# Performance work log

Measured on AMD Instinct MI355X. Metric: run time of the kernel, lower is better.

## Reference

```python
import jax, jax.numpy as jnp
import numpy as np

N_NODES = 100000
N_EDGES = 3200000
N_GRAPHS = 1024
F_IN = 78
H = 128
BN_EPS = 1e-5


def setup_inputs() -> dict:
    key = jax.random.key(0)
    ks = jax.random.split(key, 10)
    x = jax.random.normal(ks[0], (N_NODES, F_IN), dtype=jnp.float32)
    edge_index = jax.random.randint(ks[1], (2, N_EDGES), 0, N_NODES, dtype=jnp.int64)
    batch = jnp.sort(jax.random.randint(ks[2], (N_NODES,), 0, N_GRAPHS, dtype=jnp.int64))
    s_in = 1.0 / np.sqrt(F_IN)
    s_h = 1.0 / np.sqrt(H)
    return {
        "x": x,
        "edge_index": edge_index,
        "batch": batch,
        "W1_0": jax.random.normal(ks[3], (F_IN, H), dtype=jnp.float32) * s_in,
        "b1_0": jnp.zeros((H,), jnp.float32),
        "W2_0": jax.random.normal(ks[4], (H, H), dtype=jnp.float32) * s_h,
        "b2_0": jnp.zeros((H,), jnp.float32),
        "W1": jax.random.normal(ks[5], (4, H, H), dtype=jnp.float32) * s_h,
        "b1": jnp.zeros((4, H), jnp.float32),
        "W2": jax.random.normal(ks[6], (4, H, H), dtype=jnp.float32) * s_h,
        "b2": jnp.zeros((4, H), jnp.float32),
        "gamma": jnp.ones((5, H), jnp.float32),
        "beta": jnp.zeros((5, H), jnp.float32),
        "Wf": jax.random.normal(ks[7], (2 * H, H), dtype=jnp.float32) * (1.0 / np.sqrt(2 * H)),
        "bf": jnp.zeros((H,), jnp.float32),
    }


def _gin_layer(x, src, dst, W1l, b1l, W2l, b2l, g, bta):
    # GINConv, eps=0: h_i = x_i + sum_{(j->i) in E} x_j, then 2-layer MLP
    agg = jax.ops.segment_sum(x[src], dst, num_segments=N_NODES)  # [N, F]
    h = x + agg
    h = jax.nn.relu(h @ W1l + b1l) @ W2l + b2l
    h = jax.nn.relu(h)
    # BatchNorm1d (training mode: biased batch statistics)
    mu = jnp.mean(h, axis=0)
    var = jnp.mean(jnp.square(h - mu), axis=0)
    return (h - mu) * (g / jnp.sqrt(var + BN_EPS)) + bta


def reference(x, edge_index, batch, W1_0, b1_0, W2_0, b2_0, W1, b1, W2, b2, gamma, beta, Wf, bf):
    src, dst = edge_index[0], edge_index[1]
    # layer 0 (no residual: dims 78 -> 128)
    h = _gin_layer(x, src, dst, W1_0, b1_0, W2_0, b2_0, gamma[0], beta[0])
    # layers 1..4 with residual
    for i in range(4):
        h_new = _gin_layer(h, src, dst, W1[i], b1[i], W2[i], b2[i], gamma[i + 1], beta[i + 1])
        h = h + h_new
    # global mean pool
    sums = jax.ops.segment_sum(h, batch, num_segments=N_GRAPHS)  # [G, H]
    counts = jax.ops.segment_sum(jnp.ones((h.shape[0],), h.dtype), batch, num_segments=N_GRAPHS)
    mean_pool = sums / jnp.maximum(counts, 1.0)[:, None]
    # global max pool (empty segments -> 0)
    max_pool = jax.ops.segment_max(h, batch, num_segments=N_GRAPHS)
    max_pool = jnp.where(counts[:, None] > 0, max_pool, 0.0)
    combined = jnp.concatenate([mean_pool, max_pool], axis=1)  # [G, 2H]
    return combined @ Wf + bf
```

## Files before the change

kernel.cpp:

```cpp
#include <hip/hip_runtime.h>
#include <float.h>

#define N_NODES 100000
#define N_EDGES 3200000
#define N_GRAPHS 1024
#define F_IN 78
#define H 128
#define BN_EPS 1e-5f

#define BK_SHIFT 7
#define BK_NODES 128
#define NBUCKETS ((N_NODES + BK_NODES - 1) / BK_NODES)

#define P3_BLOCKS 800
#define P3_CHUNK 4000

using short8 = __attribute__((ext_vector_type(8))) short;
using f32x4v = __attribute__((ext_vector_type(4))) float;

__device__ __forceinline__ unsigned short f2bf(float f) {
    unsigned int u = __float_as_uint(f);
    unsigned int r = (u + 0x7fffu + ((u >> 16) & 1u)) >> 16;
    return (unsigned short)r;
}
__device__ __forceinline__ float bf_lo(unsigned int u) { return __uint_as_float(u << 16); }
__device__ __forceinline__ float bf_hi(unsigned int u) { return __uint_as_float(u & 0xffff0000u); }


__global__ __launch_bounds__(256) void k_hist(const int* __restrict__ dst,
                                              int* __restrict__ bofs) {
    __shared__ int lcnt[NBUCKETS];
    for (int i = threadIdx.x; i < NBUCKETS; i += 256) lcnt[i] = 0;
    __syncthreads();
    int base = blockIdx.x * P3_CHUNK;
    for (int j = threadIdx.x; j < P3_CHUNK; j += 256)
        atomicAdd(&lcnt[dst[base + j] >> BK_SHIFT], 1);
    __syncthreads();
    for (int i = threadIdx.x; i < NBUCKETS; i += 256)
        bofs[blockIdx.x * NBUCKETS + i] = lcnt[i];
}

__global__ __launch_bounds__(1024) void k_scan2(int* __restrict__ bofs,
                                                int* __restrict__ bbase,
                                                int* __restrict__ row_start) {
    __shared__ int tot[1024];
    int b = threadIdx.x;
    int run = 0;
    if (b < NBUCKETS) {
#pragma unroll 8
        for (int blk = 0; blk < P3_BLOCKS; ++blk) {
            int v = bofs[blk * NBUCKETS + b];
            bofs[blk * NBUCKETS + b] = run;
            run += v;
        }
    }
    tot[threadIdx.x] = (b < NBUCKETS) ? run : 0;
    __syncthreads();
    if (threadIdx.x == 0) {
        int acc = 0;
        for (int i = 0; i < NBUCKETS; ++i) { int t = tot[i]; tot[i] = acc; acc += t; }
    }
    __syncthreads();
    if (b < NBUCKETS) bbase[b] = tot[b];
    if (threadIdx.x == 0) {
        bbase[NBUCKETS] = N_EDGES;
        row_start[N_NODES] = N_EDGES;
    }
}

__global__ __launch_bounds__(256) void k_p3b(const int* __restrict__ src,
                                             const int* __restrict__ dst,
                                             const int* __restrict__ bofs,
                                             const int* __restrict__ bbase,
                                             unsigned int* __restrict__ ebuf) {
    __shared__ int cur[NBUCKETS];
    for (int i = threadIdx.x; i < NBUCKETS; i += 256)
        cur[i] = bbase[i] + bofs[blockIdx.x * NBUCKETS + i];
    __syncthreads();
    int base = blockIdx.x * P3_CHUNK;
    for (int j = threadIdx.x; j < P3_CHUNK; j += 256) {
        int d = dst[base + j];
        int p = atomicAdd(&cur[d >> BK_SHIFT], 1);
        ebuf[p] = ((unsigned int)src[base + j] << 7) | (unsigned int)(d & (BK_NODES - 1));
    }
}

__global__ __launch_bounds__(256) void k_p4(const int* __restrict__ bbase,
                                            const unsigned int* __restrict__ ebuf,
                                            int* __restrict__ esrc,
                                            int* __restrict__ row_start) {
    __shared__ int cur[BK_NODES];
    __shared__ int start[BK_NODES];
    int b = blockIdx.x;
    int nodeBase = b << BK_SHIFT;
    int nLocal = min(BK_NODES, N_NODES - nodeBase);
    if (threadIdx.x < BK_NODES) cur[threadIdx.x] = 0;
    __syncthreads();
    int s = bbase[b], e = bbase[b + 1];
    for (int p = s + threadIdx.x; p < e; p += 256)
        atomicAdd(&cur[ebuf[p] & (BK_NODES - 1)], 1);
    __syncthreads();
    if (threadIdx.x == 0) {
        int run = s;
        for (int i = 0; i < nLocal; ++i) { start[i] = run; run += cur[i]; }
    }
    __syncthreads();
    if (threadIdx.x < nLocal) {
        row_start[nodeBase + threadIdx.x] = start[threadIdx.x];
        cur[threadIdx.x] = start[threadIdx.x];
    }
    __syncthreads();
    for (int p = s + threadIdx.x; p < e; p += 256) {
        unsigned int ed = ebuf[p];
        int q = atomicAdd(&cur[ed & (BK_NODES - 1)], 1);
        esrc[q] = (int)(ed >> 7);
    }
}


__global__ void k_cast_x(const float* __restrict__ x, unsigned short* __restrict__ xb) {
    int i = blockIdx.x * blockDim.x + threadIdx.x;
    if (i >= N_NODES * 96) return;
    int node = i / 96;
    int c = i - node * 96;
    float v = (c < F_IN) ? x[(size_t)node * F_IN + c] : 0.f;
    xb[i] = f2bf(v);
}

__global__ void k_cast_w(const float* __restrict__ W2_0, const float* __restrict__ W1,
                         const float* __restrict__ W2, unsigned short* __restrict__ Wt) {
    int i = blockIdx.x * blockDim.x + threadIdx.x;
    if (i >= 9 * H * H) return;
    int w = i >> 14, r = i & 16383;
    int n = r >> 7, k = r & 127;
    const float* s = (w == 0) ? W2_0 : (w <= 4 ? W1 + (w - 1) * H * H : W2 + (w - 5) * H * H);
    Wt[i] = f2bf(s[k * H + n]);
}

__global__ void k_cast_w0(const float* __restrict__ W1_0, unsigned short* __restrict__ Wt0) {
    int i = blockIdx.x * blockDim.x + threadIdx.x;
    if (i >= H * 96) return;
    int n = i / 96, k = i - n * 96;
    Wt0[i] = f2bf((k < F_IN) ? W1_0[k * H + n] : 0.f);
}


__global__ void k_gather96(const unsigned int* __restrict__ xw,
                           const int* __restrict__ row_start, const int* __restrict__ esrc,
                           unsigned int* __restrict__ out) {
    int wave = threadIdx.x >> 6;
    int lane = threadIdx.x & 63;
    int node = blockIdx.x * 4 + wave;
    int s = row_start[node], e = row_start[node + 1];
    bool act = lane < 48;
    unsigned int su = act ? xw[node * 48 + lane] : 0u;
    float aA[8], aB[8];
#pragma unroll
    for (int j = 0; j < 8; ++j) { aA[j] = 0.f; aB[j] = 0.f; }
    aA[0] = bf_lo(su); aB[0] = bf_hi(su);
    int p = s;
    for (; p + 16 <= e; p += 16) {
        int idx[16];
#pragma unroll
        for (int j = 0; j < 16; ++j) idx[j] = esrc[p + j];
        unsigned int u[16];
#pragma unroll
        for (int j = 0; j < 16; ++j) u[j] = act ? xw[idx[j] * 48 + lane] : 0u;
#pragma unroll
        for (int j = 0; j < 16; ++j) { aA[j & 7] += bf_lo(u[j]); aB[j & 7] += bf_hi(u[j]); }
    }
    for (; p + 4 <= e; p += 4) {
        int i0 = esrc[p], i1 = esrc[p + 1], i2 = esrc[p + 2], i3 = esrc[p + 3];
        unsigned int u0 = act ? xw[i0 * 48 + lane] : 0u;
        unsigned int u1 = act ? xw[i1 * 48 + lane] : 0u;
        unsigned int u2 = act ? xw[i2 * 48 + lane] : 0u;
        unsigned int u3 = act ? xw[i3 * 48 + lane] : 0u;
        aA[0] += bf_lo(u0); aB[0] += bf_hi(u0); aA[1] += bf_lo(u1); aB[1] += bf_hi(u1);
        aA[2] += bf_lo(u2); aB[2] += bf_hi(u2); aA[3] += bf_lo(u3); aB[3] += bf_hi(u3);
    }
    for (; p < e; ++p) {
        unsigned int u = act ? xw[esrc[p] * 48 + lane] : 0u;
        aA[0] += bf_lo(u); aB[0] += bf_hi(u);
    }
    if (act) {
        float rx = ((aA[0] + aA[1]) + (aA[2] + aA[3])) + ((aA[4] + aA[5]) + (aA[6] + aA[7]));
        float ry = ((aB[0] + aB[1]) + (aB[2] + aB[3])) + ((aB[4] + aB[5]) + (aB[6] + aB[7]));
        out[node * 48 + lane] = (unsigned int)f2bf(rx) | ((unsigned int)f2bf(ry) << 16);
    }
}

__global__ void k_gather128b(const unsigned int* __restrict__ hw,
                             const int* __restrict__ row_start, const int* __restrict__ esrc,
                             unsigned int* __restrict__ aggb) {
    int wave = threadIdx.x >> 6;
    int lane = threadIdx.x & 63;
    int node = blockIdx.x * 4 + wave;
    int s = row_start[node], e = row_start[node + 1];
    unsigned int su = hw[node * 64 + lane];
    float aA[8], aB[8];
#pragma unroll
    for (int j = 0; j < 8; ++j) { aA[j] = 0.f; aB[j] = 0.f; }
    aA[0] = bf_lo(su); aB[0] = bf_hi(su);
    int p = s;
    for (; p + 16 <= e; p += 16) {
        int idx[16];
#pragma unroll
        for (int j = 0; j < 16; ++j) idx[j] = esrc[p + j];
        unsigned int u[16];
#pragma unroll
        for (int j = 0; j < 16; ++j) u[j] = hw[idx[j] * 64 + lane];
#pragma unroll
        for (int j = 0; j < 16; ++j) { aA[j & 7] += bf_lo(u[j]); aB[j & 7] += bf_hi(u[j]); }
    }
    for (; p + 4 <= e; p += 4) {
        int i0 = esrc[p], i1 = esrc[p + 1], i2 = esrc[p + 2], i3 = esrc[p + 3];
        unsigned int u0 = hw[i0 * 64 + lane];
        unsigned int u1 = hw[i1 * 64 + lane];
        unsigned int u2 = hw[i2 * 64 + lane];
        unsigned int u3 = hw[i3 * 64 + lane];
        aA[0] += bf_lo(u0); aB[0] += bf_hi(u0); aA[1] += bf_lo(u1); aB[1] += bf_hi(u1);
        aA[2] += bf_lo(u2); aB[2] += bf_hi(u2); aA[3] += bf_lo(u3); aB[3] += bf_hi(u3);
    }
    for (; p < e; ++p) {
        unsigned int u = hw[esrc[p] * 64 + lane];
        aA[0] += bf_lo(u); aB[0] += bf_hi(u);
    }
    float rx = ((aA[0] + aA[1]) + (aA[2] + aA[3])) + ((aA[4] + aA[5]) + (aA[6] + aA[7]));
    float ry = ((aB[0] + aB[1]) + (aB[2] + aB[3])) + ((aB[4] + aB[5]) + (aB[6] + aB[7]));
    aggb[node * 64 + lane] = (unsigned int)f2bf(rx) | ((unsigned int)f2bf(ry) << 16);
}


template <int NK>
__global__ __launch_bounds__(256) void k_mfma1t(const short* __restrict__ A,
                                                const short* __restrict__ Wt,
                                                const float* __restrict__ bias,
                                                unsigned short* __restrict__ out) {
    const int K = NK * 32;
    int wave = threadIdx.x >> 6, lane = threadIdx.x & 63;
    int r0 = blockIdx.x * 64 + wave * 16;
    int lm = lane & 15, lk = lane >> 4;
    int arow = r0 + lm;
    if (arow >= N_NODES) arow = N_NODES - 1;
    const short8* Arow = (const short8*)(A + (size_t)arow * K);
    f32x4v acc[8];
#pragma unroll
    for (int n = 0; n < 8; ++n) {
        float bv = bias[n * 16 + lm];
        acc[n] = (f32x4v){bv, bv, bv, bv};
    }
#pragma unroll
    for (int ks = 0; ks < NK; ++ks) {
        short8 af = Arow[ks * 4 + lk];
#pragma unroll
        for (int n = 0; n < 8; ++n) {
            const short8* Brow = (const short8*)(Wt + (size_t)(n * 16 + lm) * K);
            short8 bfr = Brow[ks * 4 + lk];
            acc[n] = __builtin_amdgcn_mfma_f32_16x16x32_bf16(af, bfr, acc[n], 0, 0, 0);
        }
    }
#pragma unroll
    for (int n = 0; n < 8; ++n) {
        int col = n * 16 + lm;
#pragma unroll
        for (int rg = 0; rg < 4; ++rg) {
            int r = r0 + lk * 4 + rg;
            if (r < N_NODES) {
                float v = fmaxf(acc[n][rg], 0.f);
                out[(size_t)r * H + col] = f2bf(v);
            }
        }
    }
}

__global__ __launch_bounds__(256) void k_mfma2(const short* __restrict__ A,
                                               const short* __restrict__ Wt,
                                               const float* __restrict__ bias,
                                               unsigned short* __restrict__ out,
                                               float* __restrict__ gsum,
                                               float* __restrict__ gss) {
    __shared__ float lsum[H], lss[H];
    if (threadIdx.x < H) { lsum[threadIdx.x] = 0.f; lss[threadIdx.x] = 0.f; }
    __syncthreads();
    int wave = threadIdx.x >> 6, lane = threadIdx.x & 63;
    int r0 = blockIdx.x * 64 + wave * 16;
    int lm = lane & 15, lk = lane >> 4;
    int arow = r0 + lm;
    if (arow >= N_NODES) arow = N_NODES - 1;
    const short8* Arow = (const short8*)(A + (size_t)arow * H);
    f32x4v acc[8];
#pragma unroll
    for (int n = 0; n < 8; ++n) {
        float bv = bias[n * 16 + lm];
        acc[n] = (f32x4v){bv, bv, bv, bv};
    }
#pragma unroll
    for (int ks = 0; ks < 4; ++ks) {
        short8 af = Arow[ks * 4 + lk];
#pragma unroll
        for (int n = 0; n < 8; ++n) {
            const short8* Brow = (const short8*)(Wt + (size_t)(n * 16 + lm) * H);
            short8 bfr = Brow[ks * 4 + lk];
            acc[n] = __builtin_amdgcn_mfma_f32_16x16x32_bf16(af, bfr, acc[n], 0, 0, 0);
        }
    }
#pragma unroll
    for (int n = 0; n < 8; ++n) {
        int col = n * 16 + lm;
        float s = 0.f, q = 0.f;
#pragma unroll
        for (int rg = 0; rg < 4; ++rg) {
            int r = r0 + lk * 4 + rg;
            if (r < N_NODES) {
                float v = fmaxf(acc[n][rg], 0.f);
                out[(size_t)r * H + col] = f2bf(v);
                s += v;
                q += v * v;
            }
        }
        atomicAdd(&lsum[col], s);
        atomicAdd(&lss[col], q);
    }
    __syncthreads();
    if (threadIdx.x < H) {
        atomicAdd(&gsum[threadIdx.x], lsum[threadIdx.x]);
        atomicAdd(&gss[threadIdx.x], lss[threadIdx.x]);
    }
}


__global__ void k_bnfinal(float* __restrict__ gsum, float* __restrict__ gss,
                          const float* __restrict__ gamma, const float* __restrict__ beta,
                          float* __restrict__ scale, float* __restrict__ shift) {
    int c = threadIdx.x;
    const float inv_n = 1.f / (float)N_NODES;
    float sv = gsum[c], qv = gss[c];
    gsum[c] = 0.f;
    gss[c] = 0.f;
    float mu = sv * inv_n;
    float var = fmaxf(qv * inv_n - mu * mu, 0.f);
    float sc = gamma[c] * rsqrtf(var + BN_EPS);
    scale[c] = sc;
    shift[c] = beta[c] - mu * sc;
}

template <bool RES, bool WB>
__global__ void k_bnapply(const uint2* __restrict__ vb, const float* __restrict__ scale,
                          const float* __restrict__ shift, float* __restrict__ h,
                          uint2* __restrict__ hb) {
    int idx = blockIdx.x * blockDim.x + threadIdx.x;
    if (idx >= N_NODES * H / 4) return;
    int c4 = idx & 31;
    uint2 pv = vb[idx];
    float4 val = make_float4(bf_lo(pv.x), bf_hi(pv.x), bf_lo(pv.y), bf_hi(pv.y));
    float4 sc = reinterpret_cast<const float4*>(scale)[c4];
    float4 sh = reinterpret_cast<const float4*>(shift)[c4];
    float4 r;
    r.x = val.x * sc.x + sh.x;
    r.y = val.y * sc.y + sh.y;
    r.z = val.z * sc.z + sh.z;
    r.w = val.w * sc.w + sh.w;
    if (RES) {
        float4 hv = reinterpret_cast<float4*>(h)[idx];
        r.x += hv.x; r.y += hv.y; r.z += hv.z; r.w += hv.w;
    }
    reinterpret_cast<float4*>(h)[idx] = r;
    if (WB) {
        uint2 pk;
        pk.x = (unsigned int)f2bf(r.x) | ((unsigned int)f2bf(r.y) << 16);
        pk.y = (unsigned int)f2bf(r.z) | ((unsigned int)f2bf(r.w) << 16);
        hb[idx] = pk;
    }
}


__global__ void k_bounds(const int* __restrict__ batch, int* __restrict__ row_begin) {
    int i = blockIdx.x * blockDim.x + threadIdx.x;
    if (i >= N_NODES) return;
    int bi = batch[i];
    int bp = (i == 0) ? -1 : batch[i - 1];
    for (int g = bp + 1; g <= bi; ++g) row_begin[g] = i;
    if (i == N_NODES - 1) {
        for (int g = bi + 1; g <= N_GRAPHS; ++g) row_begin[g] = N_NODES;
    }
}

__global__ void k_pool(const float* __restrict__ h, const int* __restrict__ row_begin,
                       float* __restrict__ pooled) {
    int g = blockIdx.x;
    int c = threadIdx.x;
    int s = row_begin[g], e = row_begin[g + 1];
    float sum = 0.f, mx = -FLT_MAX;
    for (int i = s; i < e; ++i) {
        float v = h[(size_t)i * H + c];
        sum += v;
        mx = fmaxf(mx, v);
    }
    int cnt = e - s;
    pooled[g * 256 + c]       = (cnt > 0) ? sum / (float)cnt : 0.f;
    pooled[g * 256 + 128 + c] = (cnt > 0) ? mx : 0.f;
}

__global__ void k_final(const float* __restrict__ pooled, const float* __restrict__ Wf,
                        const float* __restrict__ bf, float* __restrict__ out) {
    __shared__ float ps[256];
    int g = blockIdx.x, c = threadIdx.x;
    ps[c] = pooled[g * 256 + c];
    ps[128 + c] = pooled[g * 256 + 128 + c];
    __syncthreads();
    float acc = bf[c];
#pragma unroll 8
    for (int k = 0; k < 256; ++k) acc += ps[k] * Wf[k * H + c];
    out[g * H + c] = acc;
}


extern "C" void kernel_launch(void* const* d_in, const int* in_sizes, int n_in,
                              void* d_out, int out_size, void* d_ws, size_t ws_size,
                              hipStream_t stream) {
    const float* x     = (const float*)d_in[0];
    const int*   ei    = (const int*)d_in[1];
    const int*   src   = ei;
    const int*   dst   = ei + N_EDGES;
    const int*   batch = (const int*)d_in[2];
    const float* W1_0  = (const float*)d_in[3];
    const float* b1_0  = (const float*)d_in[4];
    const float* W2_0  = (const float*)d_in[5];
    const float* b2_0  = (const float*)d_in[6];
    const float* W1    = (const float*)d_in[7];
    const float* b1    = (const float*)d_in[8];
    const float* W2    = (const float*)d_in[9];
    const float* b2    = (const float*)d_in[10];
    const float* gamma = (const float*)d_in[11];
    const float* beta  = (const float*)d_in[12];
    const float* Wf    = (const float*)d_in[13];
    const float* bf    = (const float*)d_in[14];
    float* out = (float*)d_out;

    char* ws = (char*)d_ws;
    size_t off = 0;
    auto alloc = [&](size_t bytes) -> void* {
        void* p = ws + off;
        off = (off + bytes + 255) & ~(size_t)255;
        return p;
    };

    float* h    = (float*)alloc((size_t)N_NODES * H * 4);
    uint2* hb   = (uint2*)alloc((size_t)N_NODES * H * 2);
    unsigned int*   aggb  = (unsigned int*)alloc((size_t)N_NODES * H * 2);
    unsigned short* act1b = (unsigned short*)alloc((size_t)N_NODES * H * 2);
    unsigned short* act2b = (unsigned short*)alloc((size_t)N_NODES * H * 2);
    unsigned short* xb    = (unsigned short*)alloc((size_t)N_NODES * 96 * 2);
    unsigned int*   agg0b = (unsigned int*)alloc((size_t)N_NODES * 48 * 4);
    unsigned short* Wtall = (unsigned short*)alloc((size_t)9 * H * H * 2);
    unsigned short* Wt0   = (unsigned short*)alloc((size_t)H * 96 * 2);
    int* row_start = (int*)alloc((size_t)(N_NODES + 1) * 4);
    int* esrc      = (int*)alloc((size_t)N_EDGES * 4);
    unsigned int* ebuf = (unsigned int*)alloc((size_t)N_EDGES * 4);
    int* bofs      = (int*)alloc((size_t)P3_BLOCKS * NBUCKETS * 4);
    int* bbase     = (int*)alloc((size_t)(NBUCKETS + 1) * 4);
    float* gsum  = (float*)alloc(H * 4);
    float* gss   = (float*)alloc(H * 4);
    float* scale = (float*)alloc(H * 4);
    float* shift = (float*)alloc(H * 4);
    int* row_begin = (int*)alloc((size_t)(N_GRAPHS + 1) * 4);
    float* pooled  = (float*)alloc((size_t)N_GRAPHS * 256 * 4);

    k_cast_x<<<(N_NODES * 96 + 255) / 256, 256, 0, stream>>>(x, xb);
    k_cast_w<<<(9 * H * H + 255) / 256, 256, 0, stream>>>(W2_0, W1, W2, Wtall);
    k_cast_w0<<<(H * 96 + 255) / 256, 256, 0, stream>>>(W1_0, Wt0);

    k_hist<<<P3_BLOCKS, 256, 0, stream>>>(dst, bofs);
    k_scan2<<<1, 1024, 0, stream>>>(bofs, bbase, row_start);
    k_p3b<<<P3_BLOCKS, 256, 0, stream>>>(src, dst, bofs, bbase, ebuf);
    k_p4<<<NBUCKETS, 256, 0, stream>>>(bbase, ebuf, esrc, row_start);

    hipMemsetAsync(gsum, 0, H * 4, stream);
    hipMemsetAsync(gss, 0, H * 4, stream);

    const int mfma_grid = (N_NODES + 63) / 64;

    k_gather96<<<N_NODES / 4, 256, 0, stream>>>((const unsigned int*)xb, row_start, esrc, agg0b);
    k_mfma1t<3><<<mfma_grid, 256, 0, stream>>>((const short*)agg0b, (const short*)Wt0,
                                               b1_0, act1b);
    k_mfma2<<<mfma_grid, 256, 0, stream>>>((const short*)act1b, (const short*)Wtall, b2_0,
                                           act2b, gsum, gss);
    k_bnfinal<<<1, 128, 0, stream>>>(gsum, gss, gamma, beta, scale, shift);
    k_bnapply<false, true><<<N_NODES * H / 4 / 256, 256, 0, stream>>>((const uint2*)act2b,
                                                                      scale, shift, h, hb);

    for (int l = 0; l < 4; ++l) {
        k_gather128b<<<N_NODES / 4, 256, 0, stream>>>((const unsigned int*)hb, row_start,
                                                      esrc, aggb);
        k_mfma1t<4><<<mfma_grid, 256, 0, stream>>>((const short*)aggb,
                                                   (const short*)(Wtall + (1 + l) * H * H),
                                                   b1 + l * H, act1b);
        k_mfma2<<<mfma_grid, 256, 0, stream>>>((const short*)act1b,
                                               (const short*)(Wtall + (5 + l) * H * H),
                                               b2 + l * H, act2b, gsum, gss);
        k_bnfinal<<<1, 128, 0, stream>>>(gsum, gss, gamma + (l + 1) * H, beta + (l + 1) * H,
                                         scale, shift);
        if (l < 3) {
            k_bnapply<true, true><<<N_NODES * H / 4 / 256, 256, 0, stream>>>((const uint2*)act2b,
                                                                             scale, shift, h, hb);
        } else {
            k_bnapply<true, false><<<N_NODES * H / 4 / 256, 256, 0, stream>>>((const uint2*)act2b,
                                                                              scale, shift, h, hb);
        }
    }

    k_bounds<<<(N_NODES + 255) / 256, 256, 0, stream>>>(batch, row_begin);
    k_pool<<<N_GRAPHS, 128, 0, stream>>>(h, row_begin, pooled);
    k_final<<<N_GRAPHS, 128, 0, stream>>>(pooled, Wf, bf, out);
}
```

Baseline: 1.420 ms.

## Fuse MLP GEMMs via LDS, parallelize bucket scan, fold last BN into pooling

Merges the two per-layer MFMA GEMM kernels into one kernel. The ReLU'd first-layer activations stay in XOR-swizzled shared memory instead of being written to and read back from global memory. The single-block column scan is split into a many-block per-bucket scan plus a small totals scan. The final BatchNorm-apply pass is dropped and its scale/shift plus residual are applied inside the pooling kernel. The costs are 16KB more LDS per block, which may lower occupancy, and one extra kernel launch for the scan.

Result: faster. 1.272 ms (-10.4%).

```diff
diff --git a/kernel.cpp b/kernel.cpp
--- a/kernel.cpp
+++ b/kernel.cpp
@@ -25,6 +25,7 @@
 }
 __device__ __forceinline__ float bf_lo(unsigned int u) { return __uint_as_float(u << 16); }
 __device__ __forceinline__ float bf_hi(unsigned int u) { return __uint_as_float(u & 0xffff0000u); }
+__device__ __forceinline__ float bf1(unsigned short u) { return __uint_as_float((unsigned int)u << 16); }
 
 
 __global__ __launch_bounds__(256) void k_hist(const int* __restrict__ dst,
@@ -40,29 +41,50 @@
         bofs[blockIdx.x * NBUCKETS + i] = lcnt[i];
 }
 
-__global__ __launch_bounds__(1024) void k_scan2(int* __restrict__ bofs,
-                                                int* __restrict__ bbase,
-                                                int* __restrict__ row_start) {
+__global__ __launch_bounds__(256) void k_scan_a(int* __restrict__ bofs,
+                                                int* __restrict__ btot) {
+    __shared__ int part[256];
+    int b = blockIdx.x, t = threadIdx.x;
+    int val[4];
+#pragma unroll
+    for (int j = 0; j < 4; ++j) {
+        int idx = t * 4 + j;
+        val[j] = (idx < P3_BLOCKS) ? bofs[idx * NBUCKETS + b] : 0;
+    }
+    part[t] = val[0] + val[1] + val[2] + val[3];
+    __syncthreads();
+    if (t == 0) {
+        int run = 0;
+        for (int u = 0; u < 256; ++u) { int tmp = part[u]; part[u] = run; run += tmp; }
+        btot[b] = run;
+    }
+    __syncthreads();
+    int off = part[t];
+#pragma unroll
+    for (int j = 0; j < 4; ++j) {
+        int idx = t * 4 + j;
+        if (idx < P3_BLOCKS) {
+            int tmp = val[j];
+            bofs[idx * NBUCKETS + b] = off;
+            off += tmp;
+        }
+    }
+}
+
+__global__ __launch_bounds__(1024) void k_scan_b(const int* __restrict__ btot,
+                                                 int* __restrict__ bbase,
+                                                 int* __restrict__ row_start) {
     __shared__ int tot[1024];
-    int b = threadIdx.x;
-    int run = 0;
-    if (b < NBUCKETS) {
-#pragma unroll 8
-        for (int blk = 0; blk < P3_BLOCKS; ++blk) {
-            int v = bofs[blk * NBUCKETS + b];
-            bofs[blk * NBUCKETS + b] = run;
-            run += v;
-        }
-    }
-    tot[threadIdx.x] = (b < NBUCKETS) ? run : 0;
-    __syncthreads();
-    if (threadIdx.x == 0) {
+    int t = threadIdx.x;
+    tot[t] = (t < NBUCKETS) ? btot[t] : 0;
+    __syncthreads();
+    if (t == 0) {
         int acc = 0;
-        for (int i = 0; i < NBUCKETS; ++i) { int t = tot[i]; tot[i] = acc; acc += t; }
-    }
-    __syncthreads();
-    if (b < NBUCKETS) bbase[b] = tot[b];
-    if (threadIdx.x == 0) {
+        for (int i = 0; i < NBUCKETS; ++i) { int v = tot[i]; tot[i] = acc; acc += v; }
+    }
+    __syncthreads();
+    if (t < NBUCKETS) bbase[t] = tot[t];
+    if (t == 0) {
         bbase[NBUCKETS] = N_EDGES;
         row_start[N_NODES] = N_EDGES;
     }
@@ -231,88 +253,79 @@
 }
 
 
-template <int NK>
-__global__ __launch_bounds__(256) void k_mfma1t(const short* __restrict__ A,
-                                                const short* __restrict__ Wt,
-                                                const float* __restrict__ bias,
-                                                unsigned short* __restrict__ out) {
-    const int K = NK * 32;
+template <int NK1>
+__global__ __launch_bounds__(256) void k_mlp(const short* __restrict__ A,
+                                             const short* __restrict__ Wt1,
+                                             const float* __restrict__ b1v,
+                                             const short* __restrict__ Wt2,
+                                             const float* __restrict__ b2v,
+                                             unsigned short* __restrict__ out,
+                                             float* __restrict__ gsum,
+                                             float* __restrict__ gss) {
+    const int K1 = NK1 * 32;
+    __shared__ unsigned short act1[64 * H];
+    __shared__ float lsum[H], lss[H];
+    if (threadIdx.x < H) { lsum[threadIdx.x] = 0.f; lss[threadIdx.x] = 0.f; }
     int wave = threadIdx.x >> 6, lane = threadIdx.x & 63;
     int r0 = blockIdx.x * 64 + wave * 16;
     int lm = lane & 15, lk = lane >> 4;
     int arow = r0 + lm;
     if (arow >= N_NODES) arow = N_NODES - 1;
-    const short8* Arow = (const short8*)(A + (size_t)arow * K);
+    const short8* Arow = (const short8*)(A + (size_t)arow * K1);
     f32x4v acc[8];
 #pragma unroll
     for (int n = 0; n < 8; ++n) {
-        float bv = bias[n * 16 + lm];
+        float bv = b1v[n * 16 + lm];
         acc[n] = (f32x4v){bv, bv, bv, bv};
     }
 #pragma unroll
-    for (int ks = 0; ks < NK; ++ks) {
+    for (int ks = 0; ks < NK1; ++ks) {
         short8 af = Arow[ks * 4 + lk];
 #pragma unroll
         for (int n = 0; n < 8; ++n) {
-            const short8* Brow = (const short8*)(Wt + (size_t)(n * 16 + lm) * K);
+            const short8* Brow = (const short8*)(Wt1 + (size_t)(n * 16 + lm) * K1);
             short8 bfr = Brow[ks * 4 + lk];
             acc[n] = __builtin_amdgcn_mfma_f32_16x16x32_bf16(af, bfr, acc[n], 0, 0, 0);
         }
     }
 #pragma unroll
     for (int n = 0; n < 8; ++n) {
+        int colb = (n * 16 + lm) * 2;
+#pragma unroll
+        for (int rg = 0; rg < 4; ++rg) {
+            int rl = wave * 16 + lk * 4 + rg;
+            int byte = (rl * 256 + colb) ^ ((rl & 7) << 4);
+            *(unsigned short*)((char*)act1 + byte) = f2bf(fmaxf(acc[n][rg], 0.f));
+        }
+    }
+    __syncthreads();
+    f32x4v acc2[8];
+#pragma unroll
+    for (int n = 0; n < 8; ++n) {
+        float bv = b2v[n * 16 + lm];
+        acc2[n] = (f32x4v){bv, bv, bv, bv};
+    }
+    int rlr = wave * 16 + lm;
+#pragma unroll
+    for (int ks = 0; ks < 4; ++ks) {
+        int byte = (rlr * 256 + ks * 64 + lk * 16) ^ ((rlr & 7) << 4);
+        short8 af = *(const short8*)((char*)act1 + byte);
+#pragma unroll
+        for (int n = 0; n < 8; ++n) {
+            const short8* Brow = (const short8*)(Wt2 + (size_t)(n * 16 + lm) * H);
+            short8 bfr = Brow[ks * 4 + lk];
+            acc2[n] = __builtin_amdgcn_mfma_f32_16x16x32_bf16(af, bfr, acc2[n], 0, 0, 0);
+        }
+    }
+#pragma unroll
+    for (int n = 0; n < 8; ++n) {
         int col = n * 16 + lm;
+        float s = 0.f, q = 0.f;
 #pragma unroll
         for (int rg = 0; rg < 4; ++rg) {
             int r = r0 + lk * 4 + rg;
             if (r < N_NODES) {
-                float v = fmaxf(acc[n][rg], 0.f);
-                out[(size_t)r * H + col] = f2bf(v);
-            }
-        }
-    }
-}
-
-__global__ __launch_bounds__(256) void k_mfma2(const short* __restrict__ A,
-                                               const short* __restrict__ Wt,
-                                               const float* __restrict__ bias,
-                                               unsigned short* __restrict__ out,
-                                               float* __restrict__ gsum,
-                                               float* __restrict__ gss) {
-    __shared__ float lsum[H], lss[H];
-    if (threadIdx.x < H) { lsum[threadIdx.x] = 0.f; lss[threadIdx.x] = 0.f; }
-    __syncthreads();
-    int wave = threadIdx.x >> 6, lane = threadIdx.x & 63;
-    int r0 = blockIdx.x * 64 + wave * 16;
-    int lm = lane & 15, lk = lane >> 4;
-    int arow = r0 + lm;
-    if (arow >= N_NODES) arow = N_NODES - 1;
-    const short8* Arow = (const short8*)(A + (size_t)arow * H);
-    f32x4v acc[8];
-#pragma unroll
-    for (int n = 0; n < 8; ++n) {
-        float bv = bias[n * 16 + lm];
-        acc[n] = (f32x4v){bv, bv, bv, bv};
-    }
-#pragma unroll
-    for (int ks = 0; ks < 4; ++ks) {
-        short8 af = Arow[ks * 4 + lk];
-#pragma unroll
-        for (int n = 0; n < 8; ++n) {
-            const short8* Brow = (const short8*)(Wt + (size_t)(n * 16 + lm) * H);
-            short8 bfr = Brow[ks * 4 + lk];
-            acc[n] = __builtin_amdgcn_mfma_f32_16x16x32_bf16(af, bfr, acc[n], 0, 0, 0);
-        }
-    }
-#pragma unroll
-    for (int n = 0; n < 8; ++n) {
-        int col = n * 16 + lm;
-        float s = 0.f, q = 0.f;
-#pragma unroll
-        for (int rg = 0; rg < 4; ++rg) {
-            int r = r0 + lk * 4 + rg;
-            if (r < N_NODES) {
-                float v = fmaxf(acc[n][rg], 0.f);
+                float v = fmaxf(acc2[n][rg], 0.f);
                 out[(size_t)r * H + col] = f2bf(v);
                 s += v;
                 q += v * v;
@@ -385,14 +398,16 @@
     }
 }
 
-__global__ void k_pool(const float* __restrict__ h, const int* __restrict__ row_begin,
-                       float* __restrict__ pooled) {
+__global__ void k_pool_f(const unsigned short* __restrict__ act, const float* __restrict__ scale,
+                         const float* __restrict__ shift, const float* __restrict__ h3,
+                         const int* __restrict__ row_begin, float* __restrict__ pooled) {
     int g = blockIdx.x;
     int c = threadIdx.x;
+    float sc = scale[c], sh = shift[c];
     int s = row_begin[g], e = row_begin[g + 1];
     float sum = 0.f, mx = -FLT_MAX;
     for (int i = s; i < e; ++i) {
-        float v = h[(size_t)i * H + c];
+        float v = h3[(size_t)i * H + c] + sc * bf1(act[(size_t)i * H + c]) + sh;
         sum += v;
         mx = fmaxf(mx, v);
     }
@@ -448,7 +463,6 @@
     float* h    = (float*)alloc((size_t)N_NODES * H * 4);
     uint2* hb   = (uint2*)alloc((size_t)N_NODES * H * 2);
     unsigned int*   aggb  = (unsigned int*)alloc((size_t)N_NODES * H * 2);
-    unsigned short* act1b = (unsigned short*)alloc((size_t)N_NODES * H * 2);
     unsigned short* act2b = (unsigned short*)alloc((size_t)N_NODES * H * 2);
     unsigned short* xb    = (unsigned short*)alloc((size_t)N_NODES * 96 * 2);
     unsigned int*   agg0b = (unsigned int*)alloc((size_t)N_NODES * 48 * 4);
@@ -458,6 +472,7 @@
     int* esrc      = (int*)alloc((size_t)N_EDGES * 4);
     unsigned int* ebuf = (unsigned int*)alloc((size_t)N_EDGES * 4);
     int* bofs      = (int*)alloc((size_t)P3_BLOCKS * NBUCKETS * 4);
+    int* btot      = (int*)alloc((size_t)NBUCKETS * 4);
     int* bbase     = (int*)alloc((size_t)(NBUCKETS + 1) * 4);
     float* gsum  = (float*)alloc(H * 4);
     float* gss   = (float*)alloc(H * 4);
@@ -471,7 +486,8 @@
     k_cast_w0<<<(H * 96 + 255) / 256, 256, 0, stream>>>(W1_0, Wt0);
 
     k_hist<<<P3_BLOCKS, 256, 0, stream>>>(dst, bofs);
-    k_scan2<<<1, 1024, 0, stream>>>(bofs, bbase, row_start);
+    k_scan_a<<<NBUCKETS, 256, 0, stream>>>(bofs, btot);
+    k_scan_b<<<1, 1024, 0, stream>>>(btot, bbase, row_start);
     k_p3b<<<P3_BLOCKS, 256, 0, stream>>>(src, dst, bofs, bbase, ebuf);
     k_p4<<<NBUCKETS, 256, 0, stream>>>(bbase, ebuf, esrc, row_start);
 
@@ -481,10 +497,8 @@
     const int mfma_grid = (N_NODES + 63) / 64;
 
     k_gather96<<<N_NODES / 4, 256, 0, stream>>>((const unsigned int*)xb, row_start, esrc, agg0b);
-    k_mfma1t<3><<<mfma_grid, 256, 0, stream>>>((const short*)agg0b, (const short*)Wt0,
-                                               b1_0, act1b);
-    k_mfma2<<<mfma_grid, 256, 0, stream>>>((const short*)act1b, (const short*)Wtall, b2_0,
-                                           act2b, gsum, gss);
+    k_mlp<3><<<mfma_grid, 256, 0, stream>>>((const short*)agg0b, (const short*)Wt0, b1_0,
+                                            (const short*)Wtall, b2_0, act2b, gsum, gss);
     k_bnfinal<<<1, 128, 0, stream>>>(gsum, gss, gamma, beta, scale, shift);
     k_bnapply<false, true><<<N_NODES * H / 4 / 256, 256, 0, stream>>>((const uint2*)act2b,
                                                                       scale, shift, h, hb);
@@ -492,24 +506,20 @@
     for (int l = 0; l < 4; ++l) {
         k_gather128b<<<N_NODES / 4, 256, 0, stream>>>((const unsigned int*)hb, row_start,
                                                       esrc, aggb);
-        k_mfma1t<4><<<mfma_grid, 256, 0, stream>>>((const short*)aggb,
-                                                   (const short*)(Wtall + (1 + l) * H * H),
-                                                   b1 + l * H, act1b);
-        k_mfma2<<<mfma_grid, 256, 0, stream>>>((const short*)act1b,
-                                               (const short*)(Wtall + (5 + l) * H * H),
-                                               b2 + l * H, act2b, gsum, gss);
+        k_mlp<4><<<mfma_grid, 256, 0, stream>>>((const short*)aggb,
+                                                (const short*)(Wtall + (1 + l) * H * H),
+                                                b1 + l * H,
+                                                (const short*)(Wtall + (5 + l) * H * H),
+                                                b2 + l * H, act2b, gsum, gss);
         k_bnfinal<<<1, 128, 0, stream>>>(gsum, gss, gamma + (l + 1) * H, beta + (l + 1) * H,
                                          scale, shift);
         if (l < 3) {
             k_bnapply<true, true><<<N_NODES * H / 4 / 256, 256, 0, stream>>>((const uint2*)act2b,
                                                                              scale, shift, h, hb);
-        } else {
-            k_bnapply<true, false><<<N_NODES * H / 4 / 256, 256, 0, stream>>>((const uint2*)act2b,
-                                                                              scale, shift, h, hb);
         }
     }
 
     k_bounds<<<(N_NODES + 255) / 256, 256, 0, stream>>>(batch, row_begin);
-    k_pool<<<N_GRAPHS, 128, 0, stream>>>(h, row_begin, pooled);
+    k_pool_f<<<N_GRAPHS, 128, 0, stream>>>(act2b, scale, shift, h, row_begin, pooled);
     k_final<<<N_GRAPHS, 128, 0, stream>>>(pooled, Wf, bf, out);
 }
```
